# Kernel tuning notes

Measured on AMD Instinct MI355X. Metric: run time of the kernel, lower is better.

Reference implementation:

```python
import jax, jax.numpy as jnp
import numpy as np

HID = 128          # hidden_channels
NG = 256           # number of graphs in batch
NL = 50000         # ligand nodes
NP = 150000        # protein nodes
E = 500000         # edges (ligand->protein); rev edges are the reverse
RBF_COUNT = 8
D_MAX = 5.0


def _rbf(d):
    # d: [E] distances -> [E, 8] gaussian RBF expansion (D_min=0, D_max=5, count=8)
    mu = jnp.linspace(0.0, D_MAX, RBF_COUNT)
    sigma = D_MAX / RBF_COUNT
    return jnp.exp(-(((d[:, None] - mu[None, :]) / sigma) ** 2))


def setup_inputs() -> dict:
    key = jax.random.key(0)
    ks = jax.random.split(key, 24)
    s = 0.05
    inp = {
        "x_ligand": jax.random.normal(ks[0], (NL, 44), jnp.float32),
        "x_protein": jax.random.normal(ks[1], (NP, 44), jnp.float32),
        "edge_attr": jax.random.uniform(ks[2], (E, 1), jnp.float32) * D_MAX,
        "edge_src": jax.random.randint(ks[3], (E,), 0, NL),
        "edge_dst": jax.random.randint(ks[4], (E,), 0, NP),
        "ligand_batch": jnp.sort(jax.random.randint(ks[5], (NL,), 0, NG)),
        # shared node embedding and edge embedding
        "W_node": jax.random.normal(ks[6], (44, HID), jnp.float32) * s,
        "W_el": jax.random.normal(ks[7], (1, 8), jnp.float32) * s,
        # 6 NConvs: index = layer*2 + (0: ligand->protein, 1: protein->ligand)
        "Wb": jax.random.normal(ks[8], (6, RBF_COUNT, HID), jnp.float32) * s,
        "bb": jnp.zeros((6, HID), jnp.float32),
        "Wn": jax.random.normal(ks[9], (6, HID, HID), jnp.float32) * s,
        "Ws": jax.random.normal(ks[10], (6, HID, HID), jnp.float32) * s,
        "bconv": jnp.zeros((6, HID), jnp.float32),
        # edge MLP: [2*HID+8 -> 512 -> 128] (BN in eval mode = identity, dropout off)
        "W1": jax.random.normal(ks[11], (2 * HID + 8, 512), jnp.float32) * s,
        "b1": jnp.zeros((512,), jnp.float32),
        "W2": jax.random.normal(ks[12], (512, 128), jnp.float32) * s,
        "b2": jnp.zeros((128,), jnp.float32),
        # lin_mpl: 128 -> out_channels//2 = 128
        "Wm": jax.random.normal(ks[13], (128, 128), jnp.float32) * s,
        "bm": jnp.zeros((128,), jnp.float32),
    }
    return inp


def _nconv(x_src, x_dst, src, dst, n_dst, rbf_feat, Wb_i, bb_i, Wn_i, Ws_i, b_i):
    # base = SiLU(Linear(rbf)); message = fc_neigh(base * x_j); aggr = mean over dst
    base = jax.nn.silu(rbf_feat @ Wb_i + bb_i)              # [E, HID]
    msg = (base * x_src[src]) @ Wn_i                         # gather + mul + GEMM
    agg = jax.ops.segment_sum(msg, dst, num_segments=n_dst)  # [n_dst, HID]
    deg = jax.ops.segment_sum(jnp.ones((src.shape[0], 1), msg.dtype), dst,
                              num_segments=n_dst)
    agg = agg / jnp.maximum(deg, 1.0)
    return x_dst @ Ws_i + agg + b_i


def reference(x_ligand, x_protein, edge_attr, edge_src, edge_dst, ligand_batch,
              W_node, W_el, Wb, bb, Wn, Ws, bconv, W1, b1, W2, b2, Wm, bm):
    lrelu = lambda v: jax.nn.leaky_relu(v, 0.01)
    xl = x_ligand @ W_node   # [NL, HID]
    xp = x_protein @ W_node  # [NP, HID]
    rbf_feat = _rbf(jnp.squeeze(edge_attr, -1))  # [E, 8]

    xl_sum = jnp.zeros_like(xl)
    xp_sum = jnp.zeros_like(xp)
    for l in range(3):
        i_lp, i_pl = 2 * l, 2 * l + 1
        # HeteroConv applies both edge types to the SAME input dict
        xp_new = lrelu(_nconv(xl, xp, edge_src, edge_dst, NP, rbf_feat,
                              Wb[i_lp], bb[i_lp], Wn[i_lp], Ws[i_lp], bconv[i_lp]))
        xl_new = lrelu(_nconv(xp, xl, edge_dst, edge_src, NL, rbf_feat,
                              Wb[i_pl], bb[i_pl], Wn[i_pl], Ws[i_pl], bconv[i_pl]))
        xl, xp = xl_new, xp_new
        xl_sum = xl_sum + xl
        xp_sum = xp_sum + xp

    # edge readout on the ligand->protein edges
    edge_repr = jnp.concatenate([xl_sum[edge_src], xp_sum[edge_dst]], axis=-1)
    d_pl = edge_attr @ W_el                                   # [E, 8]
    edge_repr = jnp.concatenate([edge_repr, d_pl], axis=1)    # [E, 2*HID+8]
    # edge_mlp (eval mode: BatchNorm identity, dropout off)
    m_pl = jax.nn.relu(edge_repr @ W1 + b1) @ W2 + b2         # [E, 128]
    w_pl = jnp.tanh(m_pl @ Wm + bm)                           # [E, 128]
    edge_batch = ligand_batch[edge_src]
    m_w = jax.ops.segment_sum(w_pl * m_pl, edge_batch, num_segments=NG)
    m_max = jax.ops.segment_max(m_pl, edge_batch, num_segments=NG)
    m_max = jnp.where(jnp.isfinite(m_max), m_max, 0.0)        # empty segments -> 0
    return jnp.concatenate([m_w, m_max], axis=1)              # [NG, 256]
```

## Files before the change

kernel.cpp:

```cpp
#include <hip/hip_runtime.h>
#include <hip/hip_bf16.h>


#define NLn 50000
#define NPn 150000
#define En  500000
#define NBL 1563
#define NBP 4688

typedef __attribute__((ext_vector_type(8))) short short8;
typedef __attribute__((ext_vector_type(4))) float float4v;

__device__ __forceinline__ float bf2f(unsigned short u){ return __uint_as_float(((unsigned)u) << 16); }
__device__ __forceinline__ float bflo(unsigned u){ return __uint_as_float(u << 16); }
__device__ __forceinline__ float bfhi(unsigned u){ return __uint_as_float(u & 0xffff0000u); }
__device__ __forceinline__ unsigned short f2bf(float f){
  __hip_bfloat16 h = __float2bfloat16(f);
  return *reinterpret_cast<unsigned short*>(&h);
}
__device__ __forceinline__ unsigned encf(float f){
  unsigned u = __float_as_uint(f);
  return (u & 0x80000000u) ? ~u : (u | 0x80000000u);
}
__device__ __forceinline__ float tanh_fast(float x){
  return 1.f - 2.f/(__expf(2.f*x) + 1.f);
}

__global__ __launch_bounds__(256) void k_embed(
    const float* __restrict__ Xl, const float* __restrict__ Xp,
    const float* __restrict__ Wnode,
    unsigned short* __restrict__ xl0, unsigned short* __restrict__ xp0){
  __shared__ float xs[1408];
  int b = blockIdx.x, tid = threadIdx.x;
  bool isL = b < NBL;
  const float* X = isL ? Xl : Xp;
  unsigned short* out = isL ? xl0 : xp0;
  int n = isL ? NLn : NPn;
  int n0 = (isL ? b : b - NBL) * 32;
  int nrows = n - n0; if (nrows > 32) nrows = 32;
  int nflt = nrows * 44;
  const float4* Xv = (const float4*)(X + (size_t)n0*44);
  for (int j = tid; j*4 < nflt; j += 256){
    float4 v = Xv[j];
    xs[j*4+0]=v.x; xs[j*4+1]=v.y; xs[j*4+2]=v.z; xs[j*4+3]=v.w;
  }
  __syncthreads();
  int c = tid & 127, half = tid >> 7;
  float acc[16];
  #pragma unroll
  for (int r=0;r<16;r++) acc[r]=0.f;
  const float* xrow = xs + half*16*44;
  #pragma unroll 4
  for (int k=0;k<44;k++){
    float w = Wnode[k*128 + c];
    #pragma unroll
    for (int r=0;r<16;r++) acc[r] += xrow[r*44 + k] * w;
  }
  int rbase = n0 + half*16;
  #pragma unroll
  for (int r=0;r<16;r++){
    int nn = rbase + r;
    if (nn < n) out[(size_t)nn*128 + c] = f2bf(acc[r]);
  }
}

__global__ __launch_bounds__(256) void k_prep(
    unsigned* __restrict__ cntz, unsigned* __restrict__ mmaxz, unsigned* __restrict__ outz,
    const float* __restrict__ Wel, const float* __restrict__ W1, float* __restrict__ vvec,
    const float* __restrict__ W2, unsigned short* __restrict__ w2t,
    const float* __restrict__ Wm, unsigned short* __restrict__ wmt,
    const float* __restrict__ Ws, const float* __restrict__ Wn,
    unsigned short* __restrict__ wcat, unsigned short* __restrict__ w1t,
    const float* __restrict__ Wb, const float* __restrict__ bb,
    unsigned short* __restrict__ lut){
  int b = blockIdx.x, tid = threadIdx.x;
  if (b < 196){
    for (long i = (long)b*256 + tid; i < 200000; i += 196*256) cntz[i] = 0u;
  } else if (b < 324){
    mmaxz[(b-196)*256 + tid] = 0u;
  } else if (b < 580){
    outz[(b-324)*256 + tid] = 0u;
  } else if (b < 582){
    int j = (b-580)*256 + tid;
    float s = 0.f;
    #pragma unroll
    for (int r=0;r<8;r++) s += Wel[r]*W1[(256+r)*512 + j];
    vvec[j] = s;
  } else if (b < 838){
    int gid = (b-582)*256 + tid;
    int n = gid >> 9, k = gid & 511;
    w2t[n*512 + k] = f2bf(W2[k*128 + n]);
  } else if (b < 902){
    int gid = (b-838)*256 + tid;
    int n = gid >> 7, k = gid & 127;
    wmt[n*128 + k] = f2bf(Wm[k*128 + n]);
  } else if (b < 1670){
    int gid = (b-902)*256 + tid;
    int i = gid >> 15, rem = gid & 32767;
    int n = rem >> 8, k = rem & 255;
    float v = (k < 128) ? Ws[i*16384 + k*128 + n] : Wn[i*16384 + (k-128)*128 + n];
    wcat[gid] = f2bf(v);
  } else if (b < 2182){
    int gid = (b-1670)*256 + tid;
    int part = gid >> 16, rem = gid & 65535;
    int n = rem >> 7, k = rem & 127;
    w1t[gid] = f2bf(W1[(part*128 + k)*512 + n]);
  } else {
    int gid = (b-2182)*256 + tid;
    int c = gid & 127, bin = (gid >> 7) & 4095, i = gid >> 19;
    float d = ((float)bin + 0.5f) * 0.001220703125f;
    float s = bb[i*128 + c];
    #pragma unroll
    for (int j=0;j<8;j++){
      float a = (d - 0.7142857143f*(float)j) * 1.6f;
      s += __expf(-a*a) * Wb[i*1024 + j*128 + c];
    }
    lut[gid] = f2bf(s / (1.f + __expf(-s)));
  }
}

__global__ __launch_bounds__(256) void k_count(const int* __restrict__ esrc,
    const int* __restrict__ edst, unsigned* __restrict__ cntL, unsigned* __restrict__ cntP){
  int e = blockIdx.x*256 + threadIdx.x;
  if (e >= En) return;
  atomicAdd(&cntL[esrc[e]], 1u);
  atomicAdd(&cntP[edst[e]], 1u);
}
__global__ __launch_bounds__(256) void k_cs2(const unsigned* __restrict__ cntL,
    unsigned* __restrict__ rowptrL, unsigned* __restrict__ bsumL,
    const unsigned* __restrict__ cntP, unsigned* __restrict__ rowptrP,
    unsigned* __restrict__ bsumP){
  bool isL = blockIdx.x < 49;
  const unsigned* cnt = isL ? cntL : cntP;
  unsigned* rowptr = isL ? rowptrL : rowptrP;
  unsigned* bsum = isL ? bsumL : bsumP;
  int n = isL ? NLn : NPn;
  int lb = isL ? blockIdx.x : blockIdx.x - 49;
  __shared__ unsigned ts[256];
  int tid = threadIdx.x;
  int base = lb*1024 + tid*4;
  unsigned v[4], run = 0;
  #pragma unroll
  for (int j=0;j<4;j++){ v[j] = run; run += (base+j < n) ? cnt[base+j] : 0u; }
  ts[tid] = run; __syncthreads();
  for (int off=1; off<256; off<<=1){
    unsigned t = (tid>=off) ? ts[tid-off] : 0u; __syncthreads();
    ts[tid] += t; __syncthreads();
  }
  unsigned excl = ts[tid] - run;
  #pragma unroll
  for (int j=0;j<4;j++) if (base+j < n) rowptr[base+j] = excl + v[j];
  if (tid == 255) bsum[lb] = ts[255];
}
__global__ void k_sb2(unsigned* __restrict__ bsumL, unsigned* __restrict__ bsumP){
  unsigned* bsum = blockIdx.x ? bsumP : bsumL;
  int nc = blockIdx.x ? 147 : 49;
  __shared__ unsigned ts[256];
  int tid = threadIdx.x;
  unsigned x = (tid < nc) ? bsum[tid] : 0u;
  ts[tid] = x; __syncthreads();
  for (int off=1; off<256; off<<=1){
    unsigned t = (tid>=off) ? ts[tid-off] : 0u; __syncthreads();
    ts[tid] += t; __syncthreads();
  }
  if (tid < nc) bsum[tid] = ts[tid] - x;
}
__global__ __launch_bounds__(256) void k_ao2(
    unsigned* __restrict__ rowptrL, unsigned* __restrict__ cursorL,
    const unsigned* __restrict__ bsumL,
    unsigned* __restrict__ rowptrP, unsigned* __restrict__ cursorP,
    const unsigned* __restrict__ bsumP){
  bool isL = blockIdx.x < 196;
  unsigned* rowptr = isL ? rowptrL : rowptrP;
  unsigned* cursor = isL ? cursorL : cursorP;
  const unsigned* bsum = isL ? bsumL : bsumP;
  int n = isL ? NLn : NPn;
  int i = (isL ? blockIdx.x : blockIdx.x - 196)*256 + threadIdx.x;
  if (i < n){
    unsigned r = rowptr[i] + bsum[i>>10];
    rowptr[i] = r; cursor[i] = r;
  }
  if (i == 0) rowptr[n] = En;
}
__global__ __launch_bounds__(256) void k_place(const int* __restrict__ esrc,
    const int* __restrict__ edst, const float* __restrict__ ea,
    const int* __restrict__ lbatch, unsigned* __restrict__ curL,
    unsigned* __restrict__ curP, uint4* __restrict__ edgeL,
    int* __restrict__ idxL, int* __restrict__ idxP){
  int e = blockIdx.x*256 + threadIdx.x;
  if (e >= En) return;
  int s = esrc[e], d = edst[e];
  float dd = ea[e];
  int bin = (int)(dd * 819.2f);
  bin = (bin < 0) ? 0 : ((bin > 4095) ? 4095 : bin);
  unsigned pl = atomicAdd(&curL[s], 1u);
  uint4 er; er.x = (unsigned)s; er.y = (unsigned)d;
  er.z = __float_as_uint(dd); er.w = (unsigned)lbatch[s];
  edgeL[pl] = er;
  idxL[pl] = d | (bin << 18);
  unsigned pp = atomicAdd(&curP[d], 1u);
  idxP[pp] = s | (bin << 18);
}

#define EDGE_CAP 1024
__global__ __launch_bounds__(512) void k_conv2(
    const unsigned short* __restrict__ xp_in, const unsigned short* __restrict__ xl_in,
    unsigned short* __restrict__ xp_out, unsigned short* __restrict__ xl_out,
    unsigned short* __restrict__ xp_sum, unsigned short* __restrict__ xl_sum,
    const unsigned* __restrict__ rowptrP, const int* __restrict__ idxP,
    const unsigned* __restrict__ rowptrL, const int* __restrict__ idxL,
    const unsigned short* __restrict__ lut_lp,
    const unsigned short* __restrict__ wcat_lp, const float* __restrict__ bias_lp,
    const unsigned short* __restrict__ lut_pl,
    const unsigned short* __restrict__ wcat_pl, const float* __restrict__ bias_pl,
    int first){
  __shared__ unsigned short ab[32][264];
  __shared__ unsigned short ob[32][136];
  __shared__ int snb[EDGE_CAP];
  __shared__ unsigned rps[33];
  int tid = threadIdx.x;
  int c2 = tid & 63, grp = tid >> 6;
  bool isP = blockIdx.x < NBP;
  const unsigned short* xdst_in = isP ? xp_in : xl_in;
  const unsigned short* xsrc_in = isP ? xl_in : xp_in;
  unsigned short* xout = isP ? xp_out : xl_out;
  unsigned short* xsum = isP ? xp_sum : xl_sum;
  const unsigned* rowptr = isP ? rowptrP : rowptrL;
  const int* eidx = isP ? idxP : idxL;
  const unsigned short* lut_i = isP ? lut_lp : lut_pl;
  const unsigned short* wcat = isP ? wcat_lp : wcat_pl;
  const float* bias = isP ? bias_lp : bias_pl;
  int ndst = isP ? NPn : NLn;
  int n0 = (isP ? blockIdx.x : (blockIdx.x - NBP)) * 32;

  if (tid < 33){
    int idx = n0 + tid; if (idx > ndst) idx = ndst;
    rps[tid] = rowptr[idx];
  }
  __syncthreads();
  int r00 = (int)rps[0], rEnd = (int)rps[32];
  int eblk = rEnd - r00;
  bool fits = (eblk <= EDGE_CAP);
  if (fits){
    for (int p = tid; p < eblk; p += 512) snb[p] = eidx[r00 + p];
  }
  __syncthreads();

  const unsigned short* lutc = lut_i + 2*c2;
  const unsigned short* xc = xsrc_in + 2*c2;
  for (int m = grp*4; m < grp*4+4; m++){
    int n = n0 + m;
    float al0=0.f,ah0=0.f,al1=0.f,ah1=0.f,al2=0.f,ah2=0.f,al3=0.f,ah3=0.f;
    int dg = 1;
    if (n < ndst){
      *(unsigned*)&ab[m][2*c2] = *(const unsigned*)&xdst_in[(size_t)n*128 + 2*c2];
      int r0 = (int)rps[m], r1 = (int)rps[m+1];
      dg = r1 - r0;
      int p = r0;
      for (; p + 3 < r1; p += 4){
        int v0,v1,v2,v3;
        if (fits){
          v0 = snb[p-r00]; v1 = snb[p-r00+1]; v2 = snb[p-r00+2]; v3 = snb[p-r00+3];
        } else {
          v0 = eidx[p]; v1 = eidx[p+1]; v2 = eidx[p+2]; v3 = eidx[p+3];
        }
        unsigned l0 = *(const unsigned*)&lutc[(size_t)((unsigned)v0 >> 18)*128];
        unsigned x0 = *(const unsigned*)&xc[(size_t)(v0 & 0x3FFFF)*128];
        unsigned l1 = *(const unsigned*)&lutc[(size_t)((unsigned)v1 >> 18)*128];
        unsigned x1 = *(const unsigned*)&xc[(size_t)(v1 & 0x3FFFF)*128];
        unsigned l2 = *(const unsigned*)&lutc[(size_t)((unsigned)v2 >> 18)*128];
        unsigned x2 = *(const unsigned*)&xc[(size_t)(v2 & 0x3FFFF)*128];
        unsigned l3 = *(const unsigned*)&lutc[(size_t)((unsigned)v3 >> 18)*128];
        unsigned x3 = *(const unsigned*)&xc[(size_t)(v3 & 0x3FFFF)*128];
        al0 += bflo(l0)*bflo(x0); ah0 += bfhi(l0)*bfhi(x0);
        al1 += bflo(l1)*bflo(x1); ah1 += bfhi(l1)*bfhi(x1);
        al2 += bflo(l2)*bflo(x2); ah2 += bfhi(l2)*bfhi(x2);
        al3 += bflo(l3)*bflo(x3); ah3 += bfhi(l3)*bfhi(x3);
      }
      for (; p < r1; p++){
        int v0 = fits ? snb[p-r00] : eidx[p];
        unsigned l0 = *(const unsigned*)&lutc[(size_t)((unsigned)v0 >> 18)*128];
        unsigned x0 = *(const unsigned*)&xc[(size_t)(v0 & 0x3FFFF)*128];
        al0 += bflo(l0)*bflo(x0); ah0 += bfhi(l0)*bfhi(x0);
      }
    } else {
      *(unsigned*)&ab[m][2*c2] = 0u;
    }
    float inv = 1.f / (float)(dg > 1 ? dg : 1);
    float alo = ((al0+al1)+(al2+al3)) * inv;
    float ahi = ((ah0+ah1)+(ah2+ah3)) * inv;
    *(unsigned*)&ab[m][128 + 2*c2] = (unsigned)f2bf(alo) | ((unsigned)f2bf(ahi) << 16);
  }
  __syncthreads();

  int wave = tid >> 6, lane = tid & 63, quad = lane >> 4, l15 = lane & 15;
  int mt = wave & 1, nh = wave >> 1;
  int arow = mt*16 + l15;
  float4v acc[2] = {{0,0,0,0},{0,0,0,0}};
  for (int k0 = 0; k0 < 256; k0 += 32){
    short8 A = *(const short8*)&ab[arow][k0 + quad*8];
    #pragma unroll
    for (int nt=0;nt<2;nt++){
      short8 B = *(const short8*)&wcat[(size_t)(nh*32 + nt*16 + l15)*256 + k0 + quad*8];
      acc[nt] = __builtin_amdgcn_mfma_f32_16x16x32_bf16(A, B, acc[nt], 0, 0, 0);
    }
  }
  #pragma unroll
  for (int nt=0;nt<2;nt++){
    int col = nh*32 + nt*16 + l15;
    float bc = bias[col];
    #pragma unroll
    for (int r=0;r<4;r++){
      int row = mt*16 + quad*4 + r;
      float v = acc[nt][r] + bc;
      ob[row][col] = f2bf((v > 0.f) ? v : 0.01f*v);
    }
  }
  __syncthreads();
  for (int m = grp*4; m < grp*4+4; m++){
    int n = n0 + m;
    if (n < ndst){
      unsigned vb = *(unsigned*)&ob[m][2*c2];
      size_t off = (size_t)n*128 + 2*c2;
      *(unsigned*)&xout[off] = vb;
      if (first){
        *(unsigned*)&xsum[off] = vb;
      } else {
        unsigned so = *(unsigned*)&xsum[off];
        float lo = bflo(so) + bflo(vb);
        float hi = bfhi(so) + bfhi(vb);
        *(unsigned*)&xsum[off] = (unsigned)f2bf(lo) | ((unsigned)f2bf(hi) << 16);
      }
    }
  }
}

__global__ __launch_bounds__(256) void k_hproj2(
    const unsigned short* __restrict__ xl_s, const unsigned short* __restrict__ xp_s,
    const unsigned short* __restrict__ w1t, const float* __restrict__ b1,
    unsigned* __restrict__ h_l, unsigned* __restrict__ h_p){
  __shared__ unsigned short hb[32][528];
  bool isL = blockIdx.x < NBL;
  const unsigned short* xs = isL ? xl_s : xp_s;
  const unsigned short* wt = isL ? w1t : w1t + 65536;
  unsigned* hout = isL ? h_l : h_p;
  int nn = isL ? NLn : NPn;
  int n0 = (isL ? blockIdx.x : blockIdx.x - NBL)*32;
  int tid = threadIdx.x;
  int wave = tid >> 6, lane = tid & 63, quad = lane >> 4, l15 = lane & 15;
  int mt = wave & 1, nh = wave >> 1;
  int an = n0 + mt*16 + l15; if (an >= nn) an = nn - 1;
  const unsigned short* aptr = xs + (size_t)an*128;
  float4v acc[16];
  #pragma unroll
  for (int i=0;i<16;i++) acc[i] = (float4v){0,0,0,0};
  for (int k0 = 0; k0 < 128; k0 += 32){
    short8 A = *(const short8*)&aptr[k0 + quad*8];
    #pragma unroll
    for (int nt=0;nt<16;nt++){
      short8 B = *(const short8*)&wt[(size_t)(nh*256 + nt*16 + l15)*128 + k0 + quad*8];
      acc[nt] = __builtin_amdgcn_mfma_f32_16x16x32_bf16(A, B, acc[nt], 0, 0, 0);
    }
  }
  #pragma unroll
  for (int nt=0;nt<16;nt++){
    int col = nh*256 + nt*16 + l15;
    float bv = isL ? b1[col] : 0.f;
    #pragma unroll
    for (int r=0;r<4;r++) hb[mt*16 + quad*4 + r][col] = f2bf(acc[nt][r] + bv);
  }
  __syncthreads();
  for (int m=0;m<32;m++){
    int n = n0 + m;
    if (n < nn){
      unsigned pack = (unsigned)hb[m][2*tid] | ((unsigned)hb[m][2*tid+1] << 16);
      hout[(size_t)n*256 + tid] = pack;
    }
  }
}

__global__ __launch_bounds__(512) void k_readout4(
    const unsigned* __restrict__ hl, const unsigned* __restrict__ hp,
    const uint4* __restrict__ edgeL, const float* __restrict__ vvec,
    const unsigned short* __restrict__ w2t, const float* __restrict__ b2,
    const unsigned short* __restrict__ wmt, const float* __restrict__ bm,
    float* __restrict__ outw, unsigned* __restrict__ mmax){
  __shared__ __align__(16) unsigned short lds[37120];
  unsigned short (*msb)[136] = (unsigned short(*)[136])(lds + 32768);
  int tid = threadIdx.x, lane = tid & 63, wave = tid >> 6;
  int quad = lane >> 4, l15 = lane & 15;
  int ns = wave*16;

  int wg = (blockIdx.x & 7)*128 + (blockIdx.x >> 3);
  int nt_tot = En/32;
  int t0 = wg*16;
  int t1 = t0 + 16; if (t1 > nt_tot) t1 = nt_tot;
  if (t0 >= t1) return;

  short8 Bk[16];
  #pragma unroll
  for (int kk=0;kk<16;kk++)
    Bk[kk] = *(const short8*)&w2t[(size_t)(ns + l15)*512 + kk*32 + quad*8];
  short8 Bm[4];
  #pragma unroll
  for (int kk=0;kk<4;kk++)
    Bm[kk] = *(const short8*)&wmt[(size_t)(ns + l15)*128 + kk*32 + quad*8];
  float b2c0 = b2[ns + l15];
  float bm0  = bm[ns + l15];

  float4v vva = *(const float4v*)&vvec[lane*8];
  float4v vvb = *(const float4v*)&vvec[lane*8 + 4];
  int sw = lane & 31;
  const uint4* hl4 = (const uint4*)hl;
  const uint4* hp4 = (const uint4*)hp;
  const unsigned* e32 = (const unsigned*)edgeL;

  int si_prev = -1;
  uint4 ua = {0,0,0,0};
  int lm = wave*16 + (lane & 15);
  int le = lane & 31;

  #define H_EDGE(UA, UB, DD, I, WB)                                          \
    {                                                                        \
      unsigned o0,o1,o2,o3; float hx,hy;                                     \
      hx = fmaxf(bflo(UA.x)+bflo(UB.x)+(DD)*vva.x, 0.f);                     \
      hy = fmaxf(bfhi(UA.x)+bfhi(UB.x)+(DD)*vva.y, 0.f);                     \
      o0 = (unsigned)f2bf(hx) | ((unsigned)f2bf(hy) << 16);                  \
      hx = fmaxf(bflo(UA.y)+bflo(UB.y)+(DD)*vva.z, 0.f);                     \
      hy = fmaxf(bfhi(UA.y)+bfhi(UB.y)+(DD)*vva.w, 0.f);                     \
      o1 = (unsigned)f2bf(hx) | ((unsigned)f2bf(hy) << 16);                  \
      hx = fmaxf(bflo(UA.z)+bflo(UB.z)+(DD)*vvb.x, 0.f);                     \
      hy = fmaxf(bfhi(UA.z)+bfhi(UB.z)+(DD)*vvb.y, 0.f);                     \
      o2 = (unsigned)f2bf(hx) | ((unsigned)f2bf(hy) << 16);                  \
      hx = fmaxf(bflo(UA.w)+bflo(UB.w)+(DD)*vvb.z, 0.f);                     \
      hy = fmaxf(bfhi(UA.w)+bfhi(UB.w)+(DD)*vvb.w, 0.f);                     \
      o3 = (unsigned)f2bf(hx) | ((unsigned)f2bf(hy) << 16);                  \
      uint4 ov; ov.x=o0; ov.y=o1; ov.z=o2; ov.w=o3;                          \
      *(uint4*)&lds[(WB) + lane*256 + (((I) ^ sw) << 3)] = ov;               \
    }

  unsigned md1 = 0; int br_cur = 0, br1 = 0;
  {
    unsigned md0 = e32[(size_t)t0*128 + lm];
    br_cur = (int)e32[((size_t)(t0*32 + le))*4 + 3];
    #pragma unroll
    for (int ii=0; ii<4; ii++){
      int si = __builtin_amdgcn_readfirstlane(__shfl((int)md0, ii*4));
      int di = __builtin_amdgcn_readfirstlane(__shfl((int)md0, ii*4 + 1));
      float dd = __uint_as_float((unsigned)__builtin_amdgcn_readfirstlane(__shfl((int)md0, ii*4 + 2)));
      if (si != si_prev){ ua = hl4[(size_t)si*64 + lane]; si_prev = si; }
      uint4 ub = hp4[(size_t)di*64 + lane];
      H_EDGE(ua, ub, dd, wave*4 + ii, 0)
    }
    if (t0 + 1 < t1){
      md1 = e32[(size_t)(t0+1)*128 + lm];
      br1 = (int)e32[((size_t)((t0+1)*32 + le))*4 + 3];
    }
    __syncthreads();
  }

  int cur = 0;
  unsigned md2 = md1; int br2 = br1;
  for (int t = t0; t < t1; ++t){
    bool pf = (t + 1 < t1);
    if (t + 2 < t1){
      md2 = e32[(size_t)(t+2)*128 + lm];
      br2 = (int)e32[((size_t)((t+2)*32 + le))*4 + 3];
    }
    uint4 ub0, ub1, ub2, ub3;
    if (pf){
      int d0 = __builtin_amdgcn_readfirstlane(__shfl((int)md1, 1));
      int d1 = __builtin_amdgcn_readfirstlane(__shfl((int)md1, 5));
      int d2 = __builtin_amdgcn_readfirstlane(__shfl((int)md1, 9));
      int d3 = __builtin_amdgcn_readfirstlane(__shfl((int)md1, 13));
      ub0 = hp4[(size_t)d0*64 + lane];
      ub1 = hp4[(size_t)d1*64 + lane];
      ub2 = hp4[(size_t)d2*64 + lane];
      ub3 = hp4[(size_t)d3*64 + lane];
      int s0 = __builtin_amdgcn_readfirstlane(__shfl((int)md1, 0));
      if (s0 != si_prev){ ua = hl4[(size_t)s0*64 + lane]; si_prev = s0; }
    }

    int rb = cur ? 16384 : 0;
    float4v acc[2] = {{0,0,0,0},{0,0,0,0}};
    #pragma unroll
    for (int kk = 0; kk < 16; kk++){
      int kcc = kk*4 + quad;
      int sw2 = kcc & 31;
      short8 A0 = *(const short8*)&lds[rb + kcc*256 + ((l15 ^ sw2) << 3)];
      short8 A1 = *(const short8*)&lds[rb + kcc*256 + (((16 + l15) ^ sw2) << 3)];
      acc[0] = __builtin_amdgcn_mfma_f32_16x16x32_bf16(A0, Bk[kk], acc[0], 0, 0, 0);
      acc[1] = __builtin_amdgcn_mfma_f32_16x16x32_bf16(A1, Bk[kk], acc[1], 0, 0, 0);
    }
    float mreg[2][4];
    #pragma unroll
    for (int mt=0;mt<2;mt++){
      int col = ns + l15;
      #pragma unroll
      for (int r=0;r<4;r++){
        float mv = acc[mt][r] + b2c0;
        mreg[mt][r] = mv;
        msb[mt*16 + quad*4 + r][col] = f2bf(mv);
      }
    }
    __syncthreads();

    float4v acc2[2] = {{0,0,0,0},{0,0,0,0}};
    #pragma unroll
    for (int kk = 0; kk < 4; kk++){
      short8 A0 = *(const short8*)&msb[l15][kk*32 + quad*8];
      short8 A1 = *(const short8*)&msb[16 + l15][kk*32 + quad*8];
      acc2[0] = __builtin_amdgcn_mfma_f32_16x16x32_bf16(A0, Bm[kk], acc2[0], 0, 0, 0);
      acc2[1] = __builtin_amdgcn_mfma_f32_16x16x32_bf16(A1, Bm[kk], acc2[1], 0, 0, 0);
    }
    {
      int b0 = __shfl(br_cur, 0);
      bool uni = (b0 == __shfl(br_cur, 31));
      int col = ns + l15;
      if (uni){
        float s = 0.f, mx = -3.402823466e38f;
        #pragma unroll
        for (int mt=0;mt<2;mt++){
          #pragma unroll
          for (int r=0;r<4;r++){
            float mv = mreg[mt][r];
            float tt = tanh_fast(acc2[mt][r] + bm0);
            s += tt*mv; mx = fmaxf(mx, mv);
          }
        }
        s += __shfl_xor(s, 16); s += __shfl_xor(s, 32);
        mx = fmaxf(mx, __shfl_xor(mx, 16)); mx = fmaxf(mx, __shfl_xor(mx, 32));
        if (quad == 0){
          atomicAdd(&outw[b0*256 + col], s);
          atomicMax(&mmax[b0*128 + col], encf(mx));
        }
      } else {
        #pragma unroll
        for (int mt=0;mt<2;mt++){
          #pragma unroll
          for (int r=0;r<4;r++){
            int row = mt*16 + quad*4 + r;
            int b = __shfl(br_cur, row);
            float mv = mreg[mt][r];
            float tt = tanh_fast(acc2[mt][r] + bm0);
            atomicAdd(&outw[b*256 + col], tt*mv);
            atomicMax(&mmax[b*128 + col], encf(mv));
          }
        }
      }
    }

    if (pf){
      int wb = cur ? 0 : 16384;
      #pragma unroll
      for (int ii=0; ii<4; ii++){
        int si = __builtin_amdgcn_readfirstlane(__shfl((int)md1, ii*4));
        float dd = __uint_as_float((unsigned)__builtin_amdgcn_readfirstlane(__shfl((int)md1, ii*4 + 2)));
        if (si != si_prev){ ua = hl4[(size_t)si*64 + lane]; si_prev = si; }
        uint4 ub = (ii==0) ? ub0 : (ii==1) ? ub1 : (ii==2) ? ub2 : ub3;
        H_EDGE(ua, ub, dd, wave*4 + ii, wb)
      }
    }
    __syncthreads();

    md1 = md2; br_cur = br1; br1 = br2;
    cur ^= 1;
  }
  #undef H_EDGE
}

__global__ __launch_bounds__(256) void k_final(const unsigned* __restrict__ mmax,
    float* __restrict__ out){
  int gid = blockIdx.x*256 + threadIdx.x;
  unsigned enc = mmax[gid];
  float v;
  if (enc == 0u) v = 0.f;
  else if (enc & 0x80000000u) v = __uint_as_float(enc & 0x7FFFFFFFu);
  else v = __uint_as_float(~enc);
  int g = gid >> 7, cc = gid & 127;
  out[g*256 + 128 + cc] = v;
}

extern "C" void kernel_launch(void* const* d_in, const int* in_sizes, int n_in,
                              void* d_out, int out_size, void* d_ws, size_t ws_size,
                              hipStream_t stream) {
  const float* x_l    = (const float*)d_in[0];
  const float* x_p    = (const float*)d_in[1];
  const float* ea     = (const float*)d_in[2];
  const int*   esrc   = (const int*)d_in[3];
  const int*   edst   = (const int*)d_in[4];
  const int*   lbatch = (const int*)d_in[5];
  const float* W_node = (const float*)d_in[6];
  const float* W_el   = (const float*)d_in[7];
  const float* Wb     = (const float*)d_in[8];
  const float* bb     = (const float*)d_in[9];
  const float* Wn     = (const float*)d_in[10];
  const float* Ws     = (const float*)d_in[11];
  const float* bconv  = (const float*)d_in[12];
  const float* W1     = (const float*)d_in[13];
  const float* b1     = (const float*)d_in[14];
  const float* W2     = (const float*)d_in[15];
  const float* b2     = (const float*)d_in[16];
  const float* Wm     = (const float*)d_in[17];
  const float* bm     = (const float*)d_in[18];

  char* w = (char*)d_ws;
  unsigned short* xl0 = (unsigned short*)(w + 0);
  unsigned short* xl1 = (unsigned short*)(w + 12800000);
  unsigned short* xp0 = (unsigned short*)(w + 25600000);
  unsigned short* xp1 = (unsigned short*)(w + 64000000);
  int*      idxP  = (int*)(w + 102400000);
  int*      idxL  = (int*)(w + 104400000);
  unsigned short* lut = (unsigned short*)(w + 106400000);
  unsigned* h_l   = (unsigned*)(w + 0);
  unsigned* h_p   = (unsigned*)(w + 51200000);
  unsigned short* xl_s = (unsigned short*)(w + 204800000);
  unsigned short* xp_s = (unsigned short*)(w + 217600000);
  unsigned short* wcat = (unsigned short*)(w + 256000000);
  unsigned short* w1t  = (unsigned short*)(w + 256393216);
  unsigned short* w2t  = (unsigned short*)(w + 256655360);
  unsigned short* wmt  = (unsigned short*)(w + 256786432);
  float*    vvec  = (float*)(w + 256819200);
  unsigned* mmax  = (unsigned*)(w + 256821248);
  unsigned* bsumL = (unsigned*)(w + 256952320);
  unsigned* bsumP = (unsigned*)(w + 256953344);
  unsigned* rowptrL = (unsigned*)(w + 256954368);
  unsigned* cursorL = (unsigned*)(w + 257154432);
  unsigned* rowptrP = (unsigned*)(w + 257354432);
  unsigned* cursorP = (unsigned*)(w + 257954496);
  unsigned* cntL    = (unsigned*)(w + 258554496);
  unsigned* cntP    = (unsigned*)(w + 258754496);
  uint4*    edgeL   = (uint4*)(w + 259354496);

  float* out = (float*)d_out;

  k_prep<<<14470, 256, 0, stream>>>(
      (unsigned*)(w + 258554496), mmax, (unsigned*)d_out,
      W_el, W1, vvec, W2, w2t, Wm, wmt, Ws, Wn, wcat, w1t, Wb, bb, lut);
  k_embed<<<NBL + NBP, 256, 0, stream>>>(x_l, x_p, W_node, xl0, xp0);

  k_count<<<1954, 256, 0, stream>>>(esrc, edst, cntL, cntP);
  k_cs2<<<196, 256, 0, stream>>>(cntL, rowptrL, bsumL, cntP, rowptrP, bsumP);
  k_sb2<<<2, 256, 0, stream>>>(bsumL, bsumP);
  k_ao2<<<782, 256, 0, stream>>>(rowptrL, cursorL, bsumL, rowptrP, cursorP, bsumP);
  k_place<<<1954, 256, 0, stream>>>(esrc, edst, ea, lbatch, cursorL, cursorP,
                                    edgeL, idxL, idxP);

  unsigned short *xlc = xl0, *xln = xl1, *xpc = xp0, *xpn = xp1;
  for (int l = 0; l < 3; ++l){
    int ilp = 2*l, ipl = 2*l + 1;
    k_conv2<<<NBP + NBL, 512, 0, stream>>>(
        xpc, xlc, xpn, xln, xp_s, xl_s,
        rowptrP, idxP, rowptrL, idxL,
        lut + (size_t)ilp*524288, wcat + ilp*32768, bconv + ilp*128,
        lut + (size_t)ipl*524288, wcat + ipl*32768, bconv + ipl*128,
        (l == 0) ? 1 : 0);
    unsigned short* t;
    t = xlc; xlc = xln; xln = t;
    t = xpc; xpc = xpn; xpn = t;
  }

  k_hproj2<<<NBL + NBP, 256, 0, stream>>>(xl_s, xp_s, w1t, b1, h_l, h_p);

  k_readout4<<<1024, 512, 0, stream>>>(h_l, h_p, edgeL, vvec,
                                       w2t, b2, wmt, bm, out, mmax);
  k_final<<<128, 256, 0, stream>>>(mmax, out);
}
```

Baseline: 1.243 ms.

## Interleave ligand and protein blocks in conv kernel and unroll gather by eight

Block-to-work mapping in the fused conv kernel now interleaves protein and ligand destination tiles in a 3:1 pattern instead of running all protein blocks first, so the two edge directions are spread across the whole launch. The gather-accumulate loop gets an 8-wide unrolled stage that issues eight LUT and source-feature loads before accumulating, to expose more memory-level parallelism. Launch bounds also request 8 waves per SIMD occupancy. Together these aim to balance load and hide gather latency, at the risk of register pressure or spills from the wider unroll under the occupancy bound.

```diff
diff --git a/kernel.cpp b/kernel.cpp
--- a/kernel.cpp
+++ b/kernel.cpp
@@ -203,7 +203,7 @@
 }
 
 #define EDGE_CAP 1024
-__global__ __launch_bounds__(512) void k_conv2(
+__global__ __launch_bounds__(512, 8) void k_conv2(
     const unsigned short* __restrict__ xp_in, const unsigned short* __restrict__ xl_in,
     unsigned short* __restrict__ xp_out, unsigned short* __restrict__ xl_out,
     unsigned short* __restrict__ xp_sum, unsigned short* __restrict__ xl_sum,
@@ -220,7 +220,11 @@
   __shared__ unsigned rps[33];
   int tid = threadIdx.x;
   int c2 = tid & 63, grp = tid >> 6;
-  bool isP = blockIdx.x < NBP;
+  int bid = blockIdx.x;
+  bool isP; int pb;
+  if ((bid & 3) == 3){ isP = false; pb = bid >> 2; }
+  else if (bid == 6250){ isP = false; pb = 1562; }
+  else { isP = true; pb = (bid >> 2)*3 + (bid & 3); }
   const unsigned short* xdst_in = isP ? xp_in : xl_in;
   const unsigned short* xsrc_in = isP ? xl_in : xp_in;
   unsigned short* xout = isP ? xp_out : xl_out;
@@ -231,7 +235,7 @@
   const unsigned short* wcat = isP ? wcat_lp : wcat_pl;
   const float* bias = isP ? bias_lp : bias_pl;
   int ndst = isP ? NPn : NLn;
-  int n0 = (isP ? blockIdx.x : (blockIdx.x - NBP)) * 32;
+  int n0 = pb * 32;
 
   if (tid < 33){
     int idx = n0 + tid; if (idx > ndst) idx = ndst;
@@ -257,6 +261,26 @@
       int r0 = (int)rps[m], r1 = (int)rps[m+1];
       dg = r1 - r0;
       int p = r0;
+      for (; p + 7 < r1; p += 8){
+        int v[8];
+        #pragma unroll
+        for (int j=0;j<8;j++) v[j] = fits ? snb[p-r00+j] : eidx[p+j];
+        unsigned lv[8], xv[8];
+        #pragma unroll
+        for (int j=0;j<8;j++){
+          lv[j] = *(const unsigned*)&lutc[(size_t)((unsigned)v[j] >> 18)*128];
+          xv[j] = *(const unsigned*)&xc[(size_t)(v[j] & 0x3FFFF)*128];
+        }
+        #pragma unroll
+        for (int j=0;j<8;j++){
+          switch (j & 3){
+            case 0: al0 += bflo(lv[j])*bflo(xv[j]); ah0 += bfhi(lv[j])*bfhi(xv[j]); break;
+            case 1: al1 += bflo(lv[j])*bflo(xv[j]); ah1 += bfhi(lv[j])*bfhi(xv[j]); break;
+            case 2: al2 += bflo(lv[j])*bflo(xv[j]); ah2 += bfhi(lv[j])*bfhi(xv[j]); break;
+            default: al3 += bflo(lv[j])*bflo(xv[j]); ah3 += bfhi(lv[j])*bfhi(xv[j]); break;
+          }
+        }
+      }
       for (; p + 3 < r1; p += 4){
         int v0,v1,v2,v3;
         if (fits){
```

Measured after the change: 1.224 ms. About the same (-1.5%).
